# Performance work log

Measured on AMD Instinct MI355X. Metric: run time of the kernel, lower is better.

Reference implementation:

```python
import jax, jax.numpy as jnp
import numpy as np

NUM_HEADS = 16
LN_EPS = 1e-5


def setup_inputs() -> dict:
    key = jax.random.key(0)
    ks = jax.random.split(key, 5)
    B, S, E = 4, 1024, 1024
    x = jax.random.normal(ks[0], (B, S, E), dtype=jnp.float32)
    # Linear weights stored torch-style [out, in]; scaled for stable softmax
    Wq = jax.random.normal(ks[1], (E, E), dtype=jnp.float32) * (E ** -0.5)
    Wk = jax.random.normal(ks[2], (E, E), dtype=jnp.float32) * (E ** -0.5)
    Wv = jax.random.normal(ks[3], (E, E), dtype=jnp.float32) * (E ** -0.5)
    Wo = jax.random.normal(ks[4], (E, E), dtype=jnp.float32) * (E ** -0.5)
    gamma = jnp.ones((E,), dtype=jnp.float32)
    beta = jnp.zeros((E,), dtype=jnp.float32)
    return {"x": x, "Wq": Wq, "Wk": Wk, "Wv": Wv, "Wo": Wo, "gamma": gamma, "beta": beta}


def reference(x, Wq, Wk, Wv, Wo, gamma, beta):
    B, S, E = x.shape
    H = NUM_HEADS
    D = E // H
    scale = 1.0 / (D ** 0.5)

    q = x @ Wq.T                      # [B,S,E]
    k = (x @ Wk.T) * scale            # [B,S,E]
    v = x @ Wv.T                      # [B,S,E]

    qh = q.reshape(B, S, H, D)
    kh = k.reshape(B, S, H, D)
    qk = jnp.einsum('bthd,bshd->bhts', qh, kh)        # [B,H,T,S]

    causal = jnp.tril(jnp.ones((S, S), dtype=bool))   # mask==0 -> -inf
    qk = jnp.where(causal, qk, -jnp.inf)
    attn = jax.nn.softmax(qk, axis=-1)                # [B,H,T,S]

    # Faithful to torch.unflatten(v, dim=2, sizes=[-1, num_heads]):
    # heads are the LAST axis of the value split (transposed vs q/k).
    vh = v.reshape(B, S, D, H)                        # [B,S,D,H]
    # einsum 'kjlm,kmij->kiml': out[b,t,h,d] = sum_s vh[b,s,d,h]*attn[b,h,t,s]
    qkv = jnp.einsum('bsdh,bhts->bthd', vh, attn)     # [B,T,H,D]
    qkv = qkv.reshape(B, S, E)

    # LayerNorm over last dim
    mu = jnp.mean(qkv, axis=-1, keepdims=True)
    var = jnp.mean(jnp.square(qkv - mu), axis=-1, keepdims=True)
    ln = (qkv - mu) * jax.lax.rsqrt(var + LN_EPS) * gamma + beta

    return ln @ Wo.T
```

## Files before the change

### kernel.cpp

```cpp
#include <hip/hip_runtime.h>
#include <stdint.h>


using bf16x8 = __attribute__((ext_vector_type(8))) short;
using f32x4  = __attribute__((ext_vector_type(4))) float;
using u16x8  = __attribute__((ext_vector_type(8))) unsigned short;

#define AS1 __attribute__((address_space(1)))
#define AS3 __attribute__((address_space(3)))

__device__ __forceinline__ void gload16(const void* g, void* l) {
  __builtin_amdgcn_global_load_lds((const AS1 uint32_t*)g, (AS3 uint32_t*)l, 16, 0, 0);
}

__device__ __forceinline__ unsigned short f2bf(float f) {
  union { float f; uint32_t u; } v; v.f = f;
  uint32_t u = v.u + 0x7fffu + ((v.u >> 16) & 1u);
  return (unsigned short)(u >> 16);
}
__device__ __forceinline__ float bf2f(unsigned short h) {
  union { uint32_t u; float f; } v; v.u = ((uint32_t)h) << 16;
  return v.f;
}

__global__ __launch_bounds__(256) void cvt_all(const float* __restrict__ x,
                                               const float* __restrict__ Wq,
                                               const float* __restrict__ Wk,
                                               const float* __restrict__ Wv,
                                               const float* __restrict__ Wo,
                                               unsigned short* __restrict__ xb,
                                               unsigned short* __restrict__ wcat,
                                               unsigned short* __restrict__ wob) {
  int i = (int)blockIdx.x * 256 + (int)threadIdx.x;
  const float* src; unsigned short* dst; int off; float scale = 1.0f;
  if (i < 1048576)      { src = x;  dst = xb;             off = i; }
  else if (i < 1310720) { src = Wq; dst = wcat;           off = i - 1048576; }
  else if (i < 1572864) { src = Wk; dst = wcat + 1048576; off = i - 1310720; scale = 0.125f; }
  else if (i < 1835008) { src = Wv; dst = wcat + 2097152; off = i - 1572864; }
  else                  { src = Wo; dst = wob;            off = i - 1835008; }
  float4 v = reinterpret_cast<const float4*>(src)[off];
  ushort4 o;
  o.x = f2bf(v.x * scale);
  o.y = f2bf(v.y * scale);
  o.z = f2bf(v.z * scale);
  o.w = f2bf(v.w * scale);
  reinterpret_cast<ushort4*>(dst)[off] = o;
}

template<int OUTF32, int TM>
__global__ __launch_bounds__(256, 3) void gemm_bt(const unsigned short* __restrict__ A,
                                                  const unsigned short* __restrict__ B,
                                                  void* __restrict__ Cv,
                                                  int N, int K) {
  constexpr int MI = TM / 32;
  __shared__ __align__(16) unsigned short lA[2][TM * 32];
  __shared__ __align__(16) unsigned short lB[2][128 * 32];
  const int tn_cnt = N >> 7;
  const int nwg = gridDim.x;
  int bid = (int)blockIdx.x;
  int bid2 = (bid & 7) * (nwg >> 3) + (bid >> 3);
  int tm = bid2 / tn_cnt, tn = bid2 % tn_cnt;
  int t = (int)threadIdx.x;
  int w = t >> 6, lane = t & 63, lr = lane & 15, hi = lane >> 4;
  int wr = w >> 1, wc = w & 1;

  auto stage = [&](int kt, int buf) {
#pragma unroll
    for (int j = 0; j < TM / 64; ++j) {
      int ch = j * 256 + t;
      int row = ch >> 2, slot = ch & 3;
      gload16(A + (size_t)(tm * TM + row) * K + kt * 32 + ((slot ^ (row & 3)) << 3),
              (char*)lA[buf] + j * 4096 + w * 1024);
    }
#pragma unroll
    for (int j = 0; j < 2; ++j) {
      int ch = j * 256 + t;
      int row = ch >> 2, slot = ch & 3;
      gload16(B + (size_t)(tn * 128 + row) * K + kt * 32 + ((slot ^ (row & 3)) << 3),
              (char*)lB[buf] + j * 4096 + w * 1024);
    }
  };

  f32x4 acc[MI][4] = {};
  stage(0, 0);
  __syncthreads();
  const int NT = K >> 5;
  for (int kt = 0; kt < NT; ++kt) {
    int cur = kt & 1;
    if (kt + 1 < NT) stage(kt + 1, cur ^ 1);
    const char* pa = (const char*)lA[cur];
    const char* pb = (const char*)lB[cur];
    bf16x8 af[MI], bfr[4];
#pragma unroll
    for (int mi = 0; mi < MI; ++mi) {
      int row = wr * (TM / 2) + mi * 16 + lr;
      int slot = hi ^ (row & 3);
      af[mi] = *reinterpret_cast<const bf16x8*>(pa + row * 64 + slot * 16);
    }
#pragma unroll
    for (int ni = 0; ni < 4; ++ni) {
      int row = wc * 64 + ni * 16 + lr;
      int slot = hi ^ (row & 3);
      bfr[ni] = *reinterpret_cast<const bf16x8*>(pb + row * 64 + slot * 16);
    }
#pragma unroll
    for (int mi = 0; mi < MI; ++mi)
#pragma unroll
      for (int ni = 0; ni < 4; ++ni)
        acc[mi][ni] = __builtin_amdgcn_mfma_f32_16x16x32_bf16(af[mi], bfr[ni], acc[mi][ni], 0, 0, 0);
    __syncthreads();
  }
#pragma unroll
  for (int mi = 0; mi < MI; ++mi) {
#pragma unroll
    for (int r = 0; r < 4; ++r) {
      size_t row = (size_t)(tm * TM + wr * (TM / 2) + mi * 16 + hi * 4 + r);
#pragma unroll
      for (int ni = 0; ni < 4; ++ni) {
        int col = tn * 128 + wc * 64 + ni * 16 + lr;
        float v = acc[mi][ni][r];
        if (OUTF32) reinterpret_cast<float*>(Cv)[row * N + col] = v;
        else        reinterpret_cast<unsigned short*>(Cv)[row * N + col] = f2bf(v);
      }
    }
  }
}

__global__ __launch_bounds__(256) void vrepack(const unsigned short* __restrict__ QKV,
                                               unsigned short* __restrict__ VhT) {
  __shared__ __align__(16) unsigned short lT[64 * 72];
  int st = (int)blockIdx.x;
  int ct = (int)blockIdx.y;
  int b  = (int)blockIdx.z;
  int t = (int)threadIdx.x;
#pragma unroll
  for (int i = 0; i < 2; ++i) {
    int c = i * 256 + t;
    int row = c >> 3, ch = c & 7;
    u16x8 v = *reinterpret_cast<const u16x8*>(
        QKV + (size_t)(b * 1024 + st * 64 + row) * 3072 + 2048 + ct * 64 + ch * 8);
    *reinterpret_cast<u16x8*>(&lT[row * 72 + ch * 8]) = v;
  }
  __syncthreads();
#pragma unroll
  for (int i = 0; i < 2; ++i) {
    int c2 = i * 256 + t;
    int cl = c2 >> 3, ch = c2 & 7;
    int h = cl & 15;
    int d = ct * 4 + (cl >> 4);
    u16x8 v;
#pragma unroll
    for (int j = 0; j < 8; ++j) v[j] = lT[(ch * 8 + j) * 72 + cl];
    *reinterpret_cast<u16x8*>(
        VhT + (size_t)((b * 16 + h) * 64 + d) * 1024 + st * 64 + ch * 8) = v;
  }
}

__global__ __launch_bounds__(256, 2) void attn_fwd(const unsigned short* __restrict__ QKV,
                                                   const unsigned short* __restrict__ VhT,
                                                   unsigned short* __restrict__ Out) {
  __shared__ __align__(16) unsigned short lQ[128 * 64];
  __shared__ __align__(16) unsigned short lK[2][64 * 64];
  __shared__ __align__(16) unsigned short lV[2][64 * 64];
  __shared__ __align__(16) unsigned short lP[4][32 * 64];
  int bid = (int)blockIdx.x;
  int half = bid >> 8, idx = bid & 255;
  int bh = idx >> 2, jj = idx & 3;
  int qt = half ? jj : 7 - jj;
  int b = bh >> 4, h = bh & 15;
  int t = (int)threadIdx.x;
  int w = t >> 6, lane = t & 63, lr = lane & 15, hi = lane >> 4;
  (void)lane;

  auto stageKV = [&](int kb, int buf) {
#pragma unroll
    for (int i = 0; i < 2; ++i) {
      int c = i * 256 + t;
      int row = c >> 3, slot = c & 7;
      gload16(QKV + (size_t)(b * 1024 + kb * 64 + row) * 3072 + 1024 + h * 64 + ((slot ^ (row & 7)) << 3),
              (char*)lK + buf * 8192 + i * 4096 + w * 1024);
    }
#pragma unroll
    for (int i = 0; i < 2; ++i) {
      int c = i * 256 + t;
      int row = c >> 3, slot = c & 7;
      gload16(VhT + (size_t)(bh * 64 + row) * 1024 + kb * 64 + ((slot ^ (row & 7)) << 3),
              (char*)lV + buf * 8192 + i * 4096 + w * 1024);
    }
  };

#pragma unroll
  for (int i = 0; i < 4; ++i) {
    int c = i * 256 + t;
    int row = c >> 3, slot = c & 7;
    gload16(QKV + (size_t)(b * 1024 + qt * 128 + row) * 3072 + h * 64 + ((slot ^ (row & 7)) << 3),
            (char*)lQ + i * 4096 + w * 1024);
  }
  stageKV(0, 0);
  __syncthreads();

  bf16x8 qfr[2][2];
#pragma unroll
  for (int qf = 0; qf < 2; ++qf)
#pragma unroll
    for (int kc = 0; kc < 2; ++kc) {
      int row = w * 32 + qf * 16 + lr;
      int slot = (kc * 4 + hi) ^ (row & 7);
      qfr[qf][kc] = *reinterpret_cast<const bf16x8*>((const char*)lQ + row * 128 + slot * 16);
    }
  int qbase = qt * 128 + w * 32;
  f32x4 o[2][4] = {};
  float mrun[2][4], lpart[2][4];
#pragma unroll
  for (int qf = 0; qf < 2; ++qf)
#pragma unroll
    for (int r = 0; r < 4; ++r) { mrun[qf][r] = -1e30f; lpart[qf][r] = 0.f; }

  int nkb = 2 * qt + 2;
  for (int kb = 0; kb < nkb; ++kb) {
    int cur = kb & 1;
    if (kb + 1 < nkb) stageKV(kb + 1, cur ^ 1);
    if (kb * 64 <= qbase + 31) {
      const char* kbuf = (const char*)lK + cur * 8192;
      const char* vbuf = (const char*)lV + cur * 8192;
      bf16x8 kfr[4][2];
#pragma unroll
      for (int nf = 0; nf < 4; ++nf)
#pragma unroll
        for (int kc = 0; kc < 2; ++kc) {
          int row = nf * 16 + lr;
          int slot = (kc * 4 + hi) ^ (row & 7);
          kfr[nf][kc] = *reinterpret_cast<const bf16x8*>(kbuf + row * 128 + slot * 16);
        }
      f32x4 s[2][4] = {};
#pragma unroll
      for (int qf = 0; qf < 2; ++qf)
#pragma unroll
        for (int nf = 0; nf < 4; ++nf)
#pragma unroll
          for (int kc = 0; kc < 2; ++kc)
            s[qf][nf] = __builtin_amdgcn_mfma_f32_16x16x32_bf16(qfr[qf][kc], kfr[nf][kc], s[qf][nf], 0, 0, 0);
      bf16x8 vfr[4][2];
#pragma unroll
      for (int df = 0; df < 4; ++df)
#pragma unroll
        for (int kc = 0; kc < 2; ++kc) {
          int row = df * 16 + lr;
          int slot = (kc * 4 + hi) ^ (row & 7);
          vfr[df][kc] = *reinterpret_cast<const bf16x8*>(vbuf + row * 128 + slot * 16);
        }
      if (kb * 64 + 63 > qbase) {
#pragma unroll
        for (int qf = 0; qf < 2; ++qf)
#pragma unroll
          for (int nf = 0; nf < 4; ++nf)
#pragma unroll
            for (int r = 0; r < 4; ++r) {
              int q = qbase + qf * 16 + hi * 4 + r;
              int kv = kb * 64 + nf * 16 + lr;
              if (kv > q) s[qf][nf][r] = -1e30f;
            }
      }
#pragma unroll
      for (int qf = 0; qf < 2; ++qf) {
        float rm[4];
#pragma unroll
        for (int r = 0; r < 4; ++r)
          rm[r] = fmaxf(fmaxf(s[qf][0][r], s[qf][1][r]), fmaxf(s[qf][2][r], s[qf][3][r]));
#pragma unroll
        for (int r = 0; r < 4; ++r) {
          rm[r] = fmaxf(rm[r], __shfl_xor(rm[r], 1));
          rm[r] = fmaxf(rm[r], __shfl_xor(rm[r], 2));
          rm[r] = fmaxf(rm[r], __shfl_xor(rm[r], 4));
          rm[r] = fmaxf(rm[r], __shfl_xor(rm[r], 8));
        }
#pragma unroll
        for (int r = 0; r < 4; ++r) {
          float mn = fmaxf(mrun[qf][r], rm[r]);
          float al = __expf(mrun[qf][r] - mn);
          mrun[qf][r] = mn;
          float ps = 0.f;
#pragma unroll
          for (int nf = 0; nf < 4; ++nf) {
            float p = __expf(s[qf][nf][r] - mn);
            s[qf][nf][r] = p;
            ps += p;
          }
          lpart[qf][r] = lpart[qf][r] * al + ps;
#pragma unroll
          for (int df = 0; df < 4; ++df) o[qf][df][r] *= al;
        }
      }
      char* pb = (char*)lP[w];
#pragma unroll
      for (int qf = 0; qf < 2; ++qf)
#pragma unroll
        for (int nf = 0; nf < 4; ++nf)
#pragma unroll
          for (int r = 0; r < 4; ++r) {
            int rp = qf * 16 + hi * 4 + r;
            int col = nf * 16 + lr;
            int slot = (col >> 3) ^ (rp & 7);
            *reinterpret_cast<unsigned short*>(pb + rp * 128 + slot * 16 + (col & 7) * 2) =
                f2bf(s[qf][nf][r]);
          }
      asm volatile("s_waitcnt lgkmcnt(0)" ::: "memory");
      __builtin_amdgcn_sched_barrier(0);
      bf16x8 pfr[2][2];
#pragma unroll
      for (int qf = 0; qf < 2; ++qf)
#pragma unroll
        for (int kc = 0; kc < 2; ++kc) {
          int row = qf * 16 + lr;
          int slot = (kc * 4 + hi) ^ (row & 7);
          pfr[qf][kc] = *reinterpret_cast<const bf16x8*>(pb + row * 128 + slot * 16);
        }
#pragma unroll
      for (int qf = 0; qf < 2; ++qf)
#pragma unroll
        for (int df = 0; df < 4; ++df)
#pragma unroll
          for (int kc = 0; kc < 2; ++kc)
            o[qf][df] = __builtin_amdgcn_mfma_f32_16x16x32_bf16(pfr[qf][kc], vfr[df][kc], o[qf][df], 0, 0, 0);
    }
    __syncthreads();
  }

#pragma unroll
  for (int qf = 0; qf < 2; ++qf)
#pragma unroll
    for (int r = 0; r < 4; ++r) {
      float l = lpart[qf][r];
      l += __shfl_xor(l, 1);
      l += __shfl_xor(l, 2);
      l += __shfl_xor(l, 4);
      l += __shfl_xor(l, 8);
      float inv = 1.0f / l;
      int qrow = qbase + qf * 16 + hi * 4 + r;
#pragma unroll
      for (int df = 0; df < 4; ++df)
        Out[(size_t)(b * 1024 + qrow) * 1024 + h * 64 + df * 16 + lr] = f2bf(o[qf][df][r] * inv);
    }
}

__global__ __launch_bounds__(256) void lnorm(const unsigned short* __restrict__ X,
                                             unsigned short* __restrict__ Y,
                                             const float* __restrict__ gamma,
                                             const float* __restrict__ beta) {
  int rowi = (int)blockIdx.x * 4 + ((int)threadIdx.x >> 6);
  int lane = (int)threadIdx.x & 63;
  const unsigned short* row = X + (size_t)rowi * 1024;
  u16x8 v0 = reinterpret_cast<const u16x8*>(row)[lane];
  u16x8 v1 = reinterpret_cast<const u16x8*>(row)[lane + 64];
  float f0[8], f1[8];
  float s = 0.f, sq = 0.f;
#pragma unroll
  for (int j = 0; j < 8; ++j) {
    f0[j] = bf2f(v0[j]); f1[j] = bf2f(v1[j]);
    s  += f0[j] + f1[j];
    sq += f0[j] * f0[j] + f1[j] * f1[j];
  }
#pragma unroll
  for (int m = 1; m <= 32; m <<= 1) { s += __shfl_xor(s, m); sq += __shfl_xor(sq, m); }
  float mean = s * (1.0f / 1024.0f);
  float var  = sq * (1.0f / 1024.0f) - mean * mean;
  float rstd = rsqrtf(var + 1e-5f);
  int c0 = lane * 8, c1 = 512 + lane * 8;
  u16x8 o0, o1;
#pragma unroll
  for (int j = 0; j < 8; ++j) {
    o0[j] = f2bf((f0[j] - mean) * rstd * gamma[c0 + j] + beta[c0 + j]);
    o1[j] = f2bf((f1[j] - mean) * rstd * gamma[c1 + j] + beta[c1 + j]);
  }
  reinterpret_cast<u16x8*>(Y + (size_t)rowi * 1024)[lane]      = o0;
  reinterpret_cast<u16x8*>(Y + (size_t)rowi * 1024)[lane + 64] = o1;
}

extern "C" void kernel_launch(void* const* d_in, const int* in_sizes, int n_in,
                              void* d_out, int out_size, void* d_ws, size_t ws_size,
                              hipStream_t stream) {
  (void)in_sizes; (void)n_in; (void)out_size; (void)ws_size;
  const float* x     = (const float*)d_in[0];
  const float* Wq    = (const float*)d_in[1];
  const float* Wk    = (const float*)d_in[2];
  const float* Wv    = (const float*)d_in[3];
  const float* Wo    = (const float*)d_in[4];
  const float* gamma = (const float*)d_in[5];
  const float* beta  = (const float*)d_in[6];
  char* ws = (char*)d_ws;
  unsigned short* xb   = (unsigned short*)(ws);
  unsigned short* wcat = (unsigned short*)(ws + (8u  << 20));
  unsigned short* wob  = (unsigned short*)(ws + (14u << 20));
  unsigned short* qkv  = (unsigned short*)(ws + (16u << 20));
  unsigned short* vht  = (unsigned short*)(ws + (40u << 20));
  unsigned short* att  = (unsigned short*)(ws + (48u << 20));
  unsigned short* lnb  = (unsigned short*)(ws + (56u << 20));

  cvt_all<<<8192, 256, 0, stream>>>(x, Wq, Wk, Wv, Wo, xb, wcat, wob);
  gemm_bt<0, 128><<<768, 256, 0, stream>>>(xb, wcat, qkv, 3072, 1024);
  vrepack<<<dim3(16, 16, 4), 256, 0, stream>>>(qkv, vht);
  attn_fwd<<<512, 256, 0, stream>>>(qkv, vht, att);
  lnorm<<<1024, 256, 0, stream>>>(att, lnb, gamma, beta);
  gemm_bt<1, 64><<<512, 256, 0, stream>>>(lnb, wob, (void*)d_out, 1024, 1024);
}
```

Measured before the change: 186.0 us.

## Pair complementary 64-row causal query tiles per block for balanced attention work

The attention kernel now uses 64-row query tiles, each warp owning 16 rows. Each block runs two passes over tiles j and 15-j, so every block does the same number of causal KV steps. The Q buffer is also reused for the P staging area, which cuts shared memory per block. In exchange, each K/V tile loaded into LDS feeds only half as many query rows, so more K/V traffic per FLOP, and a block now does two serial passes with extra barriers.

Result: no change. 183.1 us (-1.5%).

```diff
diff --git a/kernel.cpp b/kernel.cpp
--- a/kernel.cpp
+++ b/kernel.cpp
@@ -159,14 +159,11 @@
 __global__ __launch_bounds__(256, 2) void attn_fwd(const unsigned short* __restrict__ QKV,
                                                    const unsigned short* __restrict__ VhT,
                                                    unsigned short* __restrict__ Out) {
-  __shared__ __align__(16) unsigned short lQ[128 * 64];
   __shared__ __align__(16) unsigned short lK[2][64 * 64];
   __shared__ __align__(16) unsigned short lV[2][64 * 64];
-  __shared__ __align__(16) unsigned short lP[4][32 * 64];
+  __shared__ __align__(16) unsigned short lQP[64 * 64];
   int bid = (int)blockIdx.x;
-  int half = bid >> 8, idx = bid & 255;
-  int bh = idx >> 2, jj = idx & 3;
-  int qt = half ? jj : 7 - jj;
+  int bh = bid >> 3, j = bid & 7;
   int b = bh >> 4, h = bh & 15;
   int t = (int)threadIdx.x;
   int w = t >> 6, lane = t & 63, lr = lane & 15, hi = lane >> 4;
@@ -189,38 +186,36 @@
     }
   };
 
-#pragma unroll
-  for (int i = 0; i < 4; ++i) {
-    int c = i * 256 + t;
-    int row = c >> 3, slot = c & 7;
-    gload16(QKV + (size_t)(b * 1024 + qt * 128 + row) * 3072 + h * 64 + ((slot ^ (row & 7)) << 3),
-            (char*)lQ + i * 4096 + w * 1024);
-  }
-  stageKV(0, 0);
-  __syncthreads();
-
-  bf16x8 qfr[2][2];
-#pragma unroll
-  for (int qf = 0; qf < 2; ++qf)
+#pragma unroll 1
+  for (int pass = 0; pass < 2; ++pass) {
+    int qt = pass ? (15 - j) : j;
+#pragma unroll
+    for (int i = 0; i < 2; ++i) {
+      int c = i * 256 + t;
+      int row = c >> 3, slot = c & 7;
+      gload16(QKV + (size_t)(b * 1024 + qt * 64 + row) * 3072 + h * 64 + ((slot ^ (row & 7)) << 3),
+              (char*)lQP + i * 4096 + w * 1024);
+    }
+    stageKV(0, 0);
+    __syncthreads();
+
+    bf16x8 qfr[2];
 #pragma unroll
     for (int kc = 0; kc < 2; ++kc) {
-      int row = w * 32 + qf * 16 + lr;
+      int row = w * 16 + lr;
       int slot = (kc * 4 + hi) ^ (row & 7);
-      qfr[qf][kc] = *reinterpret_cast<const bf16x8*>((const char*)lQ + row * 128 + slot * 16);
-    }
-  int qbase = qt * 128 + w * 32;
-  f32x4 o[2][4] = {};
-  float mrun[2][4], lpart[2][4];
-#pragma unroll
-  for (int qf = 0; qf < 2; ++qf)
-#pragma unroll
-    for (int r = 0; r < 4; ++r) { mrun[qf][r] = -1e30f; lpart[qf][r] = 0.f; }
-
-  int nkb = 2 * qt + 2;
-  for (int kb = 0; kb < nkb; ++kb) {
-    int cur = kb & 1;
-    if (kb + 1 < nkb) stageKV(kb + 1, cur ^ 1);
-    if (kb * 64 <= qbase + 31) {
+      qfr[kc] = *reinterpret_cast<const bf16x8*>((const char*)lQP + row * 128 + slot * 16);
+    }
+    int qbase = qt * 64 + w * 16;
+    f32x4 o[4] = {};
+    float mrun[4], lpart[4];
+#pragma unroll
+    for (int r = 0; r < 4; ++r) { mrun[r] = -1e30f; lpart[r] = 0.f; }
+
+    int nkb = qt + 1;
+    for (int kb = 0; kb < nkb; ++kb) {
+      int cur = kb & 1;
+      if (kb + 1 < nkb) stageKV(kb + 1, cur ^ 1);
       const char* kbuf = (const char*)lK + cur * 8192;
       const char* vbuf = (const char*)lV + cur * 8192;
       bf16x8 kfr[4][2];
@@ -232,14 +227,12 @@
           int slot = (kc * 4 + hi) ^ (row & 7);
           kfr[nf][kc] = *reinterpret_cast<const bf16x8*>(kbuf + row * 128 + slot * 16);
         }
-      f32x4 s[2][4] = {};
-#pragma unroll
-      for (int qf = 0; qf < 2; ++qf)
-#pragma unroll
-        for (int nf = 0; nf < 4; ++nf)
-#pragma unroll
-          for (int kc = 0; kc < 2; ++kc)
-            s[qf][nf] = __builtin_amdgcn_mfma_f32_16x16x32_bf16(qfr[qf][kc], kfr[nf][kc], s[qf][nf], 0, 0, 0);
+      f32x4 s[4] = {};
+#pragma unroll
+      for (int nf = 0; nf < 4; ++nf)
+#pragma unroll
+        for (int kc = 0; kc < 2; ++kc)
+          s[nf] = __builtin_amdgcn_mfma_f32_16x16x32_bf16(qfr[kc], kfr[nf][kc], s[nf], 0, 0, 0);
       bf16x8 vfr[4][2];
 #pragma unroll
       for (int df = 0; df < 4; ++df)
@@ -249,98 +242,86 @@
           int slot = (kc * 4 + hi) ^ (row & 7);
           vfr[df][kc] = *reinterpret_cast<const bf16x8*>(vbuf + row * 128 + slot * 16);
         }
-      if (kb * 64 + 63 > qbase) {
-#pragma unroll
-        for (int qf = 0; qf < 2; ++qf)
-#pragma unroll
-          for (int nf = 0; nf < 4; ++nf)
-#pragma unroll
-            for (int r = 0; r < 4; ++r) {
-              int q = qbase + qf * 16 + hi * 4 + r;
-              int kv = kb * 64 + nf * 16 + lr;
-              if (kv > q) s[qf][nf][r] = -1e30f;
-            }
-      }
-#pragma unroll
-      for (int qf = 0; qf < 2; ++qf) {
-        float rm[4];
-#pragma unroll
-        for (int r = 0; r < 4; ++r)
-          rm[r] = fmaxf(fmaxf(s[qf][0][r], s[qf][1][r]), fmaxf(s[qf][2][r], s[qf][3][r]));
+      if (kb == qt) {
+#pragma unroll
+        for (int nf = 0; nf < 4; ++nf)
+#pragma unroll
+          for (int r = 0; r < 4; ++r) {
+            int q = qbase + hi * 4 + r;
+            int kv = kb * 64 + nf * 16 + lr;
+            if (kv > q) s[nf][r] = -1e30f;
+          }
+      }
+      float rm[4];
+#pragma unroll
+      for (int r = 0; r < 4; ++r)
+        rm[r] = fmaxf(fmaxf(s[0][r], s[1][r]), fmaxf(s[2][r], s[3][r]));
+#pragma unroll
+      for (int r = 0; r < 4; ++r) {
+        rm[r] = fmaxf(rm[r], __shfl_xor(rm[r], 1));
+        rm[r] = fmaxf(rm[r], __shfl_xor(rm[r], 2));
+        rm[r] = fmaxf(rm[r], __shfl_xor(rm[r], 4));
+        rm[r] = fmaxf(rm[r], __shfl_xor(rm[r], 8));
+      }
+#pragma unroll
+      for (int r = 0; r < 4; ++r) {
+        float mn = fmaxf(mrun[r], rm[r]);
+        float al = __expf(mrun[r] - mn);
+        mrun[r] = mn;
+        float ps = 0.f;
+#pragma unroll
+        for (int nf = 0; nf < 4; ++nf) {
+          float p = __expf(s[nf][r] - mn);
+          s[nf][r] = p;
+          ps += p;
+        }
+        lpart[r] = lpart[r] * al + ps;
+#pragma unroll
+        for (int df = 0; df < 4; ++df) o[df][r] *= al;
+      }
+      char* pb = (char*)lQP + w * 2048;
+#pragma unroll
+      for (int nf = 0; nf < 4; ++nf)
 #pragma unroll
         for (int r = 0; r < 4; ++r) {
-          rm[r] = fmaxf(rm[r], __shfl_xor(rm[r], 1));
-          rm[r] = fmaxf(rm[r], __shfl_xor(rm[r], 2));
-          rm[r] = fmaxf(rm[r], __shfl_xor(rm[r], 4));
-          rm[r] = fmaxf(rm[r], __shfl_xor(rm[r], 8));
+          int rp = hi * 4 + r;
+          int col = nf * 16 + lr;
+          int slot = (col >> 3) ^ (rp & 7);
+          *reinterpret_cast<unsigned short*>(pb + rp * 128 + slot * 16 + (col & 7) * 2) =
+              f2bf(s[nf][r]);
         }
-#pragma unroll
-        for (int r = 0; r < 4; ++r) {
-          float mn = fmaxf(mrun[qf][r], rm[r]);
-          float al = __expf(mrun[qf][r] - mn);
-          mrun[qf][r] = mn;
-          float ps = 0.f;
-#pragma unroll
-          for (int nf = 0; nf < 4; ++nf) {
-            float p = __expf(s[qf][nf][r] - mn);
-            s[qf][nf][r] = p;
-            ps += p;
-          }
-          lpart[qf][r] = lpart[qf][r] * al + ps;
-#pragma unroll
-          for (int df = 0; df < 4; ++df) o[qf][df][r] *= al;
-        }
-      }
-      char* pb = (char*)lP[w];
-#pragma unroll
-      for (int qf = 0; qf < 2; ++qf)
-#pragma unroll
-        for (int nf = 0; nf < 4; ++nf)
-#pragma unroll
-          for (int r = 0; r < 4; ++r) {
-            int rp = qf * 16 + hi * 4 + r;
-            int col = nf * 16 + lr;
-            int slot = (col >> 3) ^ (rp & 7);
-            *reinterpret_cast<unsigned short*>(pb + rp * 128 + slot * 16 + (col & 7) * 2) =
-                f2bf(s[qf][nf][r]);
-          }
       asm volatile("s_waitcnt lgkmcnt(0)" ::: "memory");
       __builtin_amdgcn_sched_barrier(0);
-      bf16x8 pfr[2][2];
-#pragma unroll
-      for (int qf = 0; qf < 2; ++qf)
-#pragma unroll
-        for (int kc = 0; kc < 2; ++kc) {
-          int row = qf * 16 + lr;
-          int slot = (kc * 4 + hi) ^ (row & 7);
-          pfr[qf][kc] = *reinterpret_cast<const bf16x8*>(pb + row * 128 + slot * 16);
-        }
-#pragma unroll
-      for (int qf = 0; qf < 2; ++qf)
-#pragma unroll
-        for (int df = 0; df < 4; ++df)
-#pragma unroll
-          for (int kc = 0; kc < 2; ++kc)
-            o[qf][df] = __builtin_amdgcn_mfma_f32_16x16x32_bf16(pfr[qf][kc], vfr[df][kc], o[qf][df], 0, 0, 0);
-    }
-    __syncthreads();
-  }
-
-#pragma unroll
-  for (int qf = 0; qf < 2; ++qf)
+      bf16x8 pfr[2];
+#pragma unroll
+      for (int kc = 0; kc < 2; ++kc) {
+        int row = lr;
+        int slot = (kc * 4 + hi) ^ (row & 7);
+        pfr[kc] = *reinterpret_cast<const bf16x8*>(pb + row * 128 + slot * 16);
+      }
+#pragma unroll
+      for (int df = 0; df < 4; ++df)
+#pragma unroll
+        for (int kc = 0; kc < 2; ++kc)
+          o[df] = __builtin_amdgcn_mfma_f32_16x16x32_bf16(pfr[kc], vfr[df][kc], o[df], 0, 0, 0);
+      __syncthreads();
+    }
+
 #pragma unroll
     for (int r = 0; r < 4; ++r) {
-      float l = lpart[qf][r];
+      float l = lpart[r];
       l += __shfl_xor(l, 1);
       l += __shfl_xor(l, 2);
       l += __shfl_xor(l, 4);
       l += __shfl_xor(l, 8);
       float inv = 1.0f / l;
-      int qrow = qbase + qf * 16 + hi * 4 + r;
+      int qrow = qbase + hi * 4 + r;
 #pragma unroll
       for (int df = 0; df < 4; ++df)
-        Out[(size_t)(b * 1024 + qrow) * 1024 + h * 64 + df * 16 + lr] = f2bf(o[qf][df][r] * inv);
-    }
+        Out[(size_t)(b * 1024 + qrow) * 1024 + h * 64 + df * 16 + lr] = f2bf(o[df][r] * inv);
+    }
+    __syncthreads();
+  }
 }
 
 __global__ __launch_bounds__(256) void lnorm(const unsigned short* __restrict__ X,
```
